# Kernel optimization log

Measured on AMD Instinct MI355X. Metric: run time of the kernel, lower is better.

The kernel has to match this reference:

```python
import jax, jax.numpy as jnp
import numpy as np

N_NODES = 200000
N_EDGES = 6400000
IN_CH = 256
HID = 16


def gcn_conv(h, src, dst, deg_inv_sqrt, W, b, n_nodes):
    """One GCNConv (PyG semantics: add self-loops, symmetric norm, linear, scatter-add, bias)."""
    hw = h @ W  # [N, out]
    norm = deg_inv_sqrt[src] * deg_inv_sqrt[dst]  # [E]
    agg = jax.ops.segment_sum(norm[:, None] * hw[src], dst, num_segments=n_nodes)
    # self-loop contribution: deg_inv_sqrt[i]^2 * hw[i]
    agg = agg + hw * (deg_inv_sqrt ** 2)[:, None]
    return agg + b


def setup_inputs() -> dict:
    key = jax.random.key(0)
    k_x, k_e, k_w1, k_w2, k_w3 = jax.random.split(key, 5)
    x = jax.random.normal(k_x, (N_NODES, IN_CH), dtype=jnp.float32)
    edge_index = jax.random.randint(k_e, (2, N_EDGES), 0, N_NODES, dtype=jnp.int64)
    # Glorot-ish init for the three GCNConv weights, zeros for biases (PyG default)
    W1 = jax.random.normal(k_w1, (IN_CH, HID), dtype=jnp.float32) * (1.0 / np.sqrt(IN_CH))
    b1 = jnp.zeros((HID,), dtype=jnp.float32)
    W2 = jax.random.normal(k_w2, (HID, HID), dtype=jnp.float32) * (1.0 / np.sqrt(HID))
    b2 = jnp.zeros((HID,), dtype=jnp.float32)
    W3 = jax.random.normal(k_w3, (HID, 1), dtype=jnp.float32) * (1.0 / np.sqrt(HID))
    b3 = jnp.zeros((1,), dtype=jnp.float32)
    return {"x": x, "edge_index": edge_index, "W1": W1, "b1": b1,
            "W2": W2, "b2": b2, "W3": W3, "b3": b3}


def reference(x, edge_index, W1, b1, W2, b2, W3, b3):
    n_nodes = x.shape[0]
    src, dst = edge_index[0], edge_index[1]
    # GCN norm with self-loops: deg counts incoming edges + 1 self-loop
    deg = jax.ops.segment_sum(jnp.ones_like(dst, dtype=x.dtype), dst,
                              num_segments=n_nodes) + 1.0
    deg_inv_sqrt = deg ** -0.5  # deg >= 1, safe
    h = jax.nn.relu(gcn_conv(x, src, dst, deg_inv_sqrt, W1, b1, n_nodes))
    # dropout is identity in eval mode
    h = jax.nn.relu(gcn_conv(h, src, dst, deg_inv_sqrt, W2, b2, n_nodes))
    out = gcn_conv(h, src, dst, deg_inv_sqrt, W3, b3, n_nodes)  # [N, 1]
    return out
```

## Files before the change

kernel.cpp:

```cpp
#include <hip/hip_runtime.h>

#define NN 200000
#define EE 6400000L
#define NCB 196
#define CAP 36864
#define TILE 8192
#define NTILE 782
#define QSTRIDE 200064
#define GB16 12500

__device__ inline void f4add(float4& a, const float4 v) {
    a.x += v.x; a.y += v.y; a.z += v.z; a.w += v.w;
}

__global__ void k_detect(const int* __restrict__ w, int* __restrict__ flag,
                         int* __restrict__ gcur) {
    __shared__ int any;
    if (threadIdx.x == 0) any = 0;
    __syncthreads();
    int found = 0;
    for (int i = threadIdx.x; i < 8192; i += 256)
        if (w[2 * i + 1] != 0) found = 1;
    if (found) atomicOr(&any, 1);
    if (threadIdx.x < NCB) gcur[threadIdx.x] = threadIdx.x * CAP;
    __syncthreads();
    if (threadIdx.x == 0) flag[0] = any ? 0 : 1;
}

__global__ __launch_bounds__(256) void k_passA(
    const int* __restrict__ ew, const int* __restrict__ flag,
    int* __restrict__ gcur, unsigned* __restrict__ stage, long e) {
    __shared__ unsigned lv[TILE];
    __shared__ unsigned char lb[TILE];
    __shared__ int lh[NCB], lseg[NCB], lcur[NCB];
    for (int i = threadIdx.x; i < NCB; i += 256) { lh[i] = 0; lcur[i] = 0; }
    __syncthreads();
    long t0 = (long)blockIdx.x * TILE;
    int cnt = (int)min((long)TILE, e - t0);
    int shift = *flag;
    for (int i = threadIdx.x; i < cnt; i += 256) {
        int s = ew[(t0 + i) << shift];
        int d = ew[(EE + t0 + i) << shift];
        int b = d >> 10;
        lv[i] = (unsigned)s | ((unsigned)(d & 1023) << 18);
        lb[i] = (unsigned char)b;
        atomicAdd(&lh[b], 1);
    }
    __syncthreads();
    for (int i = threadIdx.x; i < NCB; i += 256)
        if (lh[i]) lseg[i] = atomicAdd(&gcur[i], lh[i]);
    __syncthreads();
    for (int i = threadIdx.x; i < cnt; i += 256) {
        int b = lb[i];
        int r = atomicAdd(&lcur[b], 1);
        stage[lseg[b] + r] = lv[i];
    }
}

__global__ __launch_bounds__(1024) void k_sortB(
    const unsigned* __restrict__ stage, const int* __restrict__ gcur,
    float* __restrict__ dis, int* __restrict__ offn, int* __restrict__ degn,
    unsigned* __restrict__ csr, int n) {
    __shared__ int cnt[1024];
    __shared__ int cur[1024];
    __shared__ int wsum[16];
    int t = threadIdx.x, B = blockIdx.x;
    cnt[t] = 0;
    __syncthreads();
    int s0 = B * CAP, s1 = gcur[B];
    for (int i = s0 + t; i < s1; i += 1024)
        atomicAdd(&cnt[stage[i] >> 18], 1);
    __syncthreads();
    int c = cnt[t];
    int lane = t & 63, w = t >> 6;
    int s = c;
#pragma unroll
    for (int o = 1; o < 64; o <<= 1) {
        int u = __shfl_up(s, o, 64);
        if (lane >= o) s += u;
    }
    if (lane == 63) wsum[w] = s;
    __syncthreads();
    int add = 0;
    for (int k = 0; k < w; ++k) add += wsum[k];
    int excl = s - c + add;
    cur[t] = excl;
    int node = B * 1024 + t;
    if (node < n) {
        offn[node] = s0 + excl;
        degn[node] = c;
        dis[node] = rsqrtf((float)(c + 1));
    }
    __syncthreads();
    for (int i = s0 + t; i < s1; i += 1024) {
        unsigned v = stage[i];
        int pos = s0 + atomicAdd(&cur[v >> 18], 1);
        csr[pos] = v & 0x3FFFF;
    }
}

__global__ __launch_bounds__(256) void k_mm1(
    const float* __restrict__ x, const float* __restrict__ W,
    const float* __restrict__ dis, float4* __restrict__ outq, int n) {
    __shared__ float Wl[256 * 16];
    int t = threadIdx.x;
#pragma unroll
    for (int i = 0; i < 4; ++i)
        ((float4*)Wl)[t + i * 256] = ((const float4*)W)[t + i * 256];
    __syncthreads();

    int node = blockIdx.x * 256 + t;
    if (node >= n) return;

    const float4* xr = (const float4*)(x + (long)node * 256);
    float acc[16];
#pragma unroll
    for (int o = 0; o < 16; ++o) acc[o] = 0.f;

#pragma unroll 8
    for (int kk = 0; kk < 64; ++kk) {
        float4 xv = xr[kk];
#pragma unroll
        for (int q = 0; q < 4; ++q) {
            float xs = (q == 0) ? xv.x : (q == 1) ? xv.y : (q == 2) ? xv.z : xv.w;
            const float4* wr = (const float4*)&Wl[(kk * 4 + q) * 16];
#pragma unroll
            for (int oo = 0; oo < 4; ++oo) {
                float4 wv = wr[oo];
                acc[oo * 4 + 0] = fmaf(xs, wv.x, acc[oo * 4 + 0]);
                acc[oo * 4 + 1] = fmaf(xs, wv.y, acc[oo * 4 + 1]);
                acc[oo * 4 + 2] = fmaf(xs, wv.z, acc[oo * 4 + 2]);
                acc[oo * 4 + 3] = fmaf(xs, wv.w, acc[oo * 4 + 3]);
            }
        }
    }
    float dv = dis[node];
#pragma unroll
    for (int q = 0; q < 4; ++q)
        outq[q * QSTRIDE + node] = make_float4(acc[q * 4] * dv, acc[q * 4 + 1] * dv,
                                               acc[q * 4 + 2] * dv, acc[q * 4 + 3] * dv);
}

__global__ __launch_bounds__(256) void k_mm2(
    const float4* __restrict__ hq, const float* __restrict__ W,
    const float* __restrict__ dis, float4* __restrict__ outq, int n) {
    __shared__ float Wl[256];
    if (threadIdx.x < 64) ((float4*)Wl)[threadIdx.x] = ((const float4*)W)[threadIdx.x];
    __syncthreads();
    int node = blockIdx.x * 256 + threadIdx.x;
    if (node >= n) return;
    float hv[16];
#pragma unroll
    for (int i = 0; i < 4; ++i) {
        float4 v = hq[i * QSTRIDE + node];
        hv[i * 4 + 0] = v.x; hv[i * 4 + 1] = v.y; hv[i * 4 + 2] = v.z; hv[i * 4 + 3] = v.w;
    }
    float acc[16];
#pragma unroll
    for (int o = 0; o < 16; ++o) acc[o] = 0.f;
#pragma unroll
    for (int k = 0; k < 16; ++k) {
        float xs = hv[k];
#pragma unroll
        for (int o = 0; o < 16; ++o) acc[o] = fmaf(xs, Wl[k * 16 + o], acc[o]);
    }
    float dv = dis[node];
#pragma unroll
    for (int q = 0; q < 4; ++q)
        outq[q * QSTRIDE + node] = make_float4(acc[q * 4] * dv, acc[q * 4 + 1] * dv,
                                               acc[q * 4 + 2] * dv, acc[q * 4 + 3] * dv);
}

__global__ __launch_bounds__(256) void k_mm3(
    const float4* __restrict__ hq, const float* __restrict__ W,
    const float* __restrict__ dis, float* __restrict__ hws3, int n) {
    int node = blockIdx.x * 256 + threadIdx.x;
    if (node >= n) return;
    float acc = 0.f;
#pragma unroll
    for (int i = 0; i < 4; ++i) {
        float4 v = hq[i * QSTRIDE + node];
        acc = fmaf(v.x, W[i * 4 + 0], acc);
        acc = fmaf(v.y, W[i * 4 + 1], acc);
        acc = fmaf(v.z, W[i * 4 + 2], acc);
        acc = fmaf(v.w, W[i * 4 + 3], acc);
    }
    hws3[node] = acc * dis[node];
}

template <int RELU>
__global__ __launch_bounds__(256) void k_g16p(
    const int* __restrict__ offn, const int* __restrict__ degn,
    const unsigned* __restrict__ csr, const float* __restrict__ dis,
    const float4* __restrict__ tabq, const float* __restrict__ b,
    float4* __restrict__ outq, int n) {
    int bid = blockIdx.x;
    int q = bid / GB16;
    int g = bid - q * GB16;
    int t = threadIdx.x;
    int node = g * 16 + (t >> 4);
    int ln = t & 15;
    if (node >= n) return;
    const float4* tab = tabq + (long)q * QSTRIDE;
    int s0 = offn[node], dg = degn[node];
    float4 a0 = make_float4(0.f, 0.f, 0.f, 0.f);
    float4 a1 = make_float4(0.f, 0.f, 0.f, 0.f);
    int k = ln;
    for (; k + 16 < dg; k += 32) {
        f4add(a0, tab[csr[s0 + k]]);
        f4add(a1, tab[csr[s0 + k + 16]]);
    }
    if (k < dg) f4add(a0, tab[csr[s0 + k]]);
    f4add(a0, a1);
#pragma unroll
    for (int o = 8; o >= 1; o >>= 1) {
        a0.x += __shfl_xor(a0.x, o, 16);
        a0.y += __shfl_xor(a0.y, o, 16);
        a0.z += __shfl_xor(a0.z, o, 16);
        a0.w += __shfl_xor(a0.w, o, 16);
    }
    if (ln == 0) {
        f4add(a0, tab[node]);
        float dv = dis[node];
        float4 bb = ((const float4*)b)[q];
        float4 r = make_float4(fmaf(dv, a0.x, bb.x), fmaf(dv, a0.y, bb.y),
                               fmaf(dv, a0.z, bb.z), fmaf(dv, a0.w, bb.w));
        if (RELU) {
            r.x = fmaxf(r.x, 0.f); r.y = fmaxf(r.y, 0.f);
            r.z = fmaxf(r.z, 0.f); r.w = fmaxf(r.w, 0.f);
        }
        outq[(long)q * QSTRIDE + node] = r;
    }
}

__global__ __launch_bounds__(256) void k_g1(
    const int* __restrict__ offn, const int* __restrict__ degn,
    const unsigned* __restrict__ csr, const float* __restrict__ dis,
    const float* __restrict__ hws3, const float* __restrict__ b,
    float* __restrict__ out, int n) {
    int t = threadIdx.x;
    int node = blockIdx.x * 16 + (t >> 4);
    int ln = t & 15;
    if (node >= n) return;
    int s0 = offn[node], dg = degn[node];
    float acc = 0.f;
    for (int k = ln; k < dg; k += 16)
        acc += hws3[csr[s0 + k]];
#pragma unroll
    for (int o = 8; o >= 1; o >>= 1) acc += __shfl_down(acc, o, 16);
    if (ln == 0)
        out[node] = fmaf(dis[node], acc + hws3[node], b[0]);
}

extern "C" void kernel_launch(void* const* d_in, const int* in_sizes, int n_in,
                              void* d_out, int out_size, void* d_ws, size_t ws_size,
                              hipStream_t stream) {
    const float* x  = (const float*)d_in[0];
    const int*   ew = (const int*)d_in[1];
    const float* W1 = (const float*)d_in[2];
    const float* b1 = (const float*)d_in[3];
    const float* W2 = (const float*)d_in[4];
    const float* b2 = (const float*)d_in[5];
    const float* W3 = (const float*)d_in[6];
    const float* b3 = (const float*)d_in[7];
    float* out = (float*)d_out;

    unsigned* stage = (unsigned*)d_ws;
    unsigned* csr   = stage + (long)NCB * CAP;
    int*      gcur  = (int*)(csr + (long)NCB * CAP);
    int*      flag  = gcur + 256;
    int*      offn  = flag + 16;
    int*      degn  = offn + 200704;
    float*    dis   = (float*)(degn + 200704);
    float4*   bufA  = (float4*)(dis + 200704);
    float4*   bufB  = bufA + 4 * QSTRIDE;

    const int n = NN;
    const long e = EE;
    int nb = (n + 255) / 256;
    int g1b = (n + 15) / 16;

    k_detect<<<1, 256, 0, stream>>>(ew, flag, gcur);
    k_passA<<<NTILE, 256, 0, stream>>>(ew, flag, gcur, stage, e);
    k_sortB<<<NCB, 1024, 0, stream>>>(stage, gcur, dis, offn, degn, csr, n);

    k_mm1<<<nb, 256, 0, stream>>>(x, W1, dis, bufA, n);
    k_g16p<1><<<4 * GB16, 256, 0, stream>>>(offn, degn, csr, dis, bufA, b1, bufB, n);
    k_mm2<<<nb, 256, 0, stream>>>(bufB, W2, dis, bufA, n);
    k_g16p<1><<<4 * GB16, 256, 0, stream>>>(offn, degn, csr, dis, bufA, b2, bufB, n);
    k_mm3<<<nb, 256, 0, stream>>>(bufB, W3, dis, (float*)bufA, n);
    k_g1<<<g1b, 256, 0, stream>>>(offn, degn, csr, dis, (const float*)bufA, b3, out, n);
}
```

Measured before the change: 499.7 us.

## Pad CSR rows to multiples of four and gather with 4-lane vector index loads

Each node's CSR segment is padded to a multiple of four entries so the gather kernel can read indices as aligned uint4 loads. Each node now uses 4 lanes instead of 16, with two accumulators and a short scalar tail handled by one lane. Offset and degree are packed into a single int2 array. The aim is fewer index load instructions and less shuffle-reduction overhead, at the cost of fewer lanes per node, which may expose latency for high-degree nodes. The padding must still fit inside the per-bucket CAP region.

```diff
diff --git a/kernel.cpp b/kernel.cpp
--- a/kernel.cpp
+++ b/kernel.cpp
@@ -7,7 +7,7 @@
 #define TILE 8192
 #define NTILE 782
 #define QSTRIDE 200064
-#define GB16 12500
+#define GB64 3125
 
 __device__ inline void f4add(float4& a, const float4 v) {
     a.x += v.x; a.y += v.y; a.z += v.z; a.w += v.w;
@@ -59,7 +59,7 @@
 
 __global__ __launch_bounds__(1024) void k_sortB(
     const unsigned* __restrict__ stage, const int* __restrict__ gcur,
-    float* __restrict__ dis, int* __restrict__ offn, int* __restrict__ degn,
+    float* __restrict__ dis, int2* __restrict__ odn,
     unsigned* __restrict__ csr, int n) {
     __shared__ int cnt[1024];
     __shared__ int cur[1024];
@@ -72,8 +72,9 @@
         atomicAdd(&cnt[stage[i] >> 18], 1);
     __syncthreads();
     int c = cnt[t];
+    int pc = (c + 3) & ~3;
     int lane = t & 63, w = t >> 6;
-    int s = c;
+    int s = pc;
 #pragma unroll
     for (int o = 1; o < 64; o <<= 1) {
         int u = __shfl_up(s, o, 64);
@@ -83,12 +84,11 @@
     __syncthreads();
     int add = 0;
     for (int k = 0; k < w; ++k) add += wsum[k];
-    int excl = s - c + add;
+    int excl = s - pc + add;
     cur[t] = excl;
     int node = B * 1024 + t;
     if (node < n) {
-        offn[node] = s0 + excl;
-        degn[node] = c;
+        odn[node] = make_int2(s0 + excl, c);
         dis[node] = rsqrtf((float)(c + 1));
     }
     __syncthreads();
@@ -189,42 +189,54 @@
 }
 
 template <int RELU>
-__global__ __launch_bounds__(256) void k_g16p(
-    const int* __restrict__ offn, const int* __restrict__ degn,
-    const unsigned* __restrict__ csr, const float* __restrict__ dis,
-    const float4* __restrict__ tabq, const float* __restrict__ b,
-    float4* __restrict__ outq, int n) {
+__global__ __launch_bounds__(256) void k_g16q(
+    const int2* __restrict__ odn, const unsigned* __restrict__ csr,
+    const float* __restrict__ dis, const float4* __restrict__ tabq,
+    const float* __restrict__ b, float4* __restrict__ outq, int n) {
     int bid = blockIdx.x;
-    int q = bid / GB16;
-    int g = bid - q * GB16;
+    int q = bid / GB64;
+    int g = bid - q * GB64;
     int t = threadIdx.x;
-    int node = g * 16 + (t >> 4);
-    int ln = t & 15;
+    int node = g * 64 + (t >> 2);
+    int j = t & 3;
     if (node >= n) return;
     const float4* tab = tabq + (long)q * QSTRIDE;
-    int s0 = offn[node], dg = degn[node];
-    float4 a0 = make_float4(0.f, 0.f, 0.f, 0.f);
-    float4 a1 = make_float4(0.f, 0.f, 0.f, 0.f);
-    int k = ln;
-    for (; k + 16 < dg; k += 32) {
-        f4add(a0, tab[csr[s0 + k]]);
-        f4add(a1, tab[csr[s0 + k + 16]]);
-    }
-    if (k < dg) f4add(a0, tab[csr[s0 + k]]);
-    f4add(a0, a1);
-#pragma unroll
-    for (int o = 8; o >= 1; o >>= 1) {
-        a0.x += __shfl_xor(a0.x, o, 16);
-        a0.y += __shfl_xor(a0.y, o, 16);
-        a0.z += __shfl_xor(a0.z, o, 16);
-        a0.w += __shfl_xor(a0.w, o, 16);
-    }
-    if (ln == 0) {
-        f4add(a0, tab[node]);
+    int2 od = odn[node];
+    int s0 = od.x, dg = od.y;
+    float4 aA = make_float4(0.f, 0.f, 0.f, 0.f);
+    float4 aB = make_float4(0.f, 0.f, 0.f, 0.f);
+    int c0 = 4 * j;
+    for (; c0 + 20 <= dg; c0 += 32) {
+        uint4 eL = *(const uint4*)(csr + s0 + c0);
+        uint4 eH = *(const uint4*)(csr + s0 + c0 + 16);
+        f4add(aA, tab[eL.x]); f4add(aB, tab[eH.x]);
+        f4add(aA, tab[eL.y]); f4add(aB, tab[eH.y]);
+        f4add(aA, tab[eL.z]); f4add(aB, tab[eH.z]);
+        f4add(aA, tab[eL.w]); f4add(aB, tab[eH.w]);
+    }
+    for (; c0 + 4 <= dg; c0 += 16) {
+        uint4 e = *(const uint4*)(csr + s0 + c0);
+        f4add(aA, tab[e.x]); f4add(aA, tab[e.y]);
+        f4add(aA, tab[e.z]); f4add(aA, tab[e.w]);
+    }
+    if ((dg & 3) && j == ((dg >> 2) & 3)) {
+        for (int k2 = dg & ~3; k2 < dg; ++k2)
+            f4add(aA, tab[csr[s0 + k2]]);
+    }
+    f4add(aA, aB);
+#pragma unroll
+    for (int o = 1; o <= 2; o <<= 1) {
+        aA.x += __shfl_xor(aA.x, o, 4);
+        aA.y += __shfl_xor(aA.y, o, 4);
+        aA.z += __shfl_xor(aA.z, o, 4);
+        aA.w += __shfl_xor(aA.w, o, 4);
+    }
+    if (j == 0) {
+        f4add(aA, tab[node]);
         float dv = dis[node];
         float4 bb = ((const float4*)b)[q];
-        float4 r = make_float4(fmaf(dv, a0.x, bb.x), fmaf(dv, a0.y, bb.y),
-                               fmaf(dv, a0.z, bb.z), fmaf(dv, a0.w, bb.w));
+        float4 r = make_float4(fmaf(dv, aA.x, bb.x), fmaf(dv, aA.y, bb.y),
+                               fmaf(dv, aA.z, bb.z), fmaf(dv, aA.w, bb.w));
         if (RELU) {
             r.x = fmaxf(r.x, 0.f); r.y = fmaxf(r.y, 0.f);
             r.z = fmaxf(r.z, 0.f); r.w = fmaxf(r.w, 0.f);
@@ -234,15 +246,15 @@
 }
 
 __global__ __launch_bounds__(256) void k_g1(
-    const int* __restrict__ offn, const int* __restrict__ degn,
-    const unsigned* __restrict__ csr, const float* __restrict__ dis,
-    const float* __restrict__ hws3, const float* __restrict__ b,
-    float* __restrict__ out, int n) {
+    const int2* __restrict__ odn, const unsigned* __restrict__ csr,
+    const float* __restrict__ dis, const float* __restrict__ hws3,
+    const float* __restrict__ b, float* __restrict__ out, int n) {
     int t = threadIdx.x;
     int node = blockIdx.x * 16 + (t >> 4);
     int ln = t & 15;
     if (node >= n) return;
-    int s0 = offn[node], dg = degn[node];
+    int2 od = odn[node];
+    int s0 = od.x, dg = od.y;
     float acc = 0.f;
     for (int k = ln; k < dg; k += 16)
         acc += hws3[csr[s0 + k]];
@@ -269,9 +281,8 @@
     unsigned* csr   = stage + (long)NCB * CAP;
     int*      gcur  = (int*)(csr + (long)NCB * CAP);
     int*      flag  = gcur + 256;
-    int*      offn  = flag + 16;
-    int*      degn  = offn + 200704;
-    float*    dis   = (float*)(degn + 200704);
+    int2*     odn   = (int2*)(flag + 16);
+    float*    dis   = (float*)(odn + 200704);
     float4*   bufA  = (float4*)(dis + 200704);
     float4*   bufB  = bufA + 4 * QSTRIDE;
 
@@ -282,12 +293,12 @@
 
     k_detect<<<1, 256, 0, stream>>>(ew, flag, gcur);
     k_passA<<<NTILE, 256, 0, stream>>>(ew, flag, gcur, stage, e);
-    k_sortB<<<NCB, 1024, 0, stream>>>(stage, gcur, dis, offn, degn, csr, n);
+    k_sortB<<<NCB, 1024, 0, stream>>>(stage, gcur, dis, odn, csr, n);
 
     k_mm1<<<nb, 256, 0, stream>>>(x, W1, dis, bufA, n);
-    k_g16p<1><<<4 * GB16, 256, 0, stream>>>(offn, degn, csr, dis, bufA, b1, bufB, n);
+    k_g16q<1><<<4 * GB64, 256, 0, stream>>>(odn, csr, dis, bufA, b1, bufB, n);
     k_mm2<<<nb, 256, 0, stream>>>(bufB, W2, dis, bufA, n);
-    k_g16p<1><<<4 * GB16, 256, 0, stream>>>(offn, degn, csr, dis, bufA, b2, bufB, n);
+    k_g16q<1><<<4 * GB64, 256, 0, stream>>>(odn, csr, dis, bufA, b2, bufB, n);
     k_mm3<<<nb, 256, 0, stream>>>(bufB, W3, dis, (float*)bufA, n);
-    k_g1<<<g1b, 256, 0, stream>>>(offn, degn, csr, dis, (const float*)bufA, b3, out, n);
-}
+    k_g1<<<g1b, 256, 0, stream>>>(odn, csr, dis, (const float*)bufA, b3, out, n);
+}
```

After: 524.3 us (median of 6 runs). 4.9% more time.
